# Performance work log

Hardware: AMD Instinct MI355X
Metric: run time of the kernel (lower is better)

## Reference

```python
import jax, jax.numpy as jnp
import numpy as np

B, S, HIDDEN = 2, 2048, 1024
HEADS, HEAD_DIM = 16, 64
GRID_SIZE, SPLINE_ORDER = 5, 3  # efficient-kan defaults


def b_splines(x, grid, k=SPLINE_ORDER):
    """x: (N, in), grid: (in, GRID_SIZE + 2k + 1) -> (N, in, GRID_SIZE + k)."""
    xe = x[..., None]
    bases = ((xe >= grid[:, :-1]) & (xe < grid[:, 1:])).astype(x.dtype)
    for p in range(1, k + 1):  # Cox-de Boor recursion, fixed small loop
        left = (xe - grid[:, : -(p + 1)]) / (grid[:, p:-1] - grid[:, : -(p + 1)]) * bases[..., :-1]
        right = (grid[:, p + 1:] - xe) / (grid[:, p + 1:] - grid[:, 1:-p]) * bases[..., 1:]
        bases = left + right
    return bases


def setup_inputs() -> dict:
    key = jax.random.key(0)
    ks = jax.random.split(key, 7)
    h = 2.0 / GRID_SIZE  # grid_range = [-1, 1]
    grid_1d = (jnp.arange(-SPLINE_ORDER, GRID_SIZE + SPLINE_ORDER + 1, dtype=jnp.float32) * h - 1.0)
    grid = jnp.tile(grid_1d[None, :], (HIDDEN, 1))  # (in, 12)
    return {
        "x": jax.random.normal(ks[0], (B, S, HIDDEN), jnp.float32),
        "base_weight": jax.random.normal(ks[1], (3 * HIDDEN, HIDDEN), jnp.float32) * 0.02,
        "spline_weight": jax.random.normal(ks[2], (3 * HIDDEN, HIDDEN, GRID_SIZE + SPLINE_ORDER), jnp.float32) * 0.02,
        "spline_scaler": jax.random.normal(ks[3], (3 * HIDDEN, HIDDEN), jnp.float32) * 0.1 + 1.0,
        "grid": grid,
        "rotation_matrix": jax.random.normal(ks[4], (HEAD_DIM, HEAD_DIM), jnp.float32) / np.sqrt(HEAD_DIM),
        "out_w": jax.random.normal(ks[5], (HIDDEN, HIDDEN), jnp.float32) * 0.02,
        "out_b": jnp.zeros((HIDDEN,), jnp.float32),
    }


def reference(x, base_weight, spline_weight, spline_scaler, grid, rotation_matrix, out_w, out_b):
    Bc, Sc, Hc = x.shape
    xf = x.reshape(-1, Hc)  # (N, in)
    # KANLinear: silu base branch + B-spline branch
    base = jax.nn.silu(xf) @ base_weight.T  # (N, 3H)
    bs = b_splines(xf, grid)  # (N, in, G+k)
    sw = spline_weight * spline_scaler[..., None]  # scaled spline weight
    spline = bs.reshape(bs.shape[0], -1) @ sw.reshape(sw.shape[0], -1).T
    qkv = (base + spline).reshape(Bc, Sc, HEADS, 3 * HEAD_DIM).transpose(0, 2, 1, 3)
    q, k, v = jnp.split(qkv, 3, axis=-1)  # each (B,H,S,dh)
    # RoPE via full learned rotation matrix
    qr = jnp.einsum('bhsd,md->bhsm', q, rotation_matrix)
    kr = jnp.einsum('bhsd,md->bhsm', k, rotation_matrix)
    scores = jnp.einsum('bhsm,bhtm->bhst', qr, kr) / (HEAD_DIM ** 0.5)
    attn = jax.nn.softmax(scores, axis=-1)
    ctx = jnp.einsum('bhst,bhtd->bhsd', attn, v)
    ctx = ctx.transpose(0, 2, 1, 3).reshape(Bc, Sc, Hc)
    return ctx @ out_w.T + out_b
```

## Files before the change

kernel.cpp:

```cpp
#include <hip/hip_runtime.h>
#include <cstdint>
#include <cstddef>

typedef __bf16 bf16;
typedef bf16  bf16x8 __attribute__((ext_vector_type(8)));
typedef float f32x4  __attribute__((ext_vector_type(4)));

#define GLOBAL_AS __attribute__((address_space(1)))
#define LDS_AS    __attribute__((address_space(3)))

__device__ __forceinline__ void ldg_lds16(const void* g, void* l) {
  __builtin_amdgcn_global_load_lds((const GLOBAL_AS void*)g, (LDS_AS void*)l, 16, 0, 0);
}

constexpr int NB    = 2;
constexpr int SQ    = 2048;
constexpr int HID   = 1024;
constexpr int NHEAD = 16;
constexpr int HD    = 64;
constexpr int NROW  = NB * SQ;
constexpr int KA    = HID + HID * 8;
constexpr int NO    = 3 * HID;

constexpr int NBW = NO * (KA / 8) / 256;
constexpr int NBA = NROW * HID / 256;
constexpr int NBC = HID * HID / 1024;

__global__ __launch_bounds__(256) void prep(const float* __restrict__ X,
                                            const float* __restrict__ Grid,
                                            const float* __restrict__ BW,
                                            const float* __restrict__ SW,
                                            const float* __restrict__ SS,
                                            const float* __restrict__ OW,
                                            bf16* __restrict__ A,
                                            bf16* __restrict__ Wp,
                                            bf16* __restrict__ WOB) {
  const int bx = blockIdx.x, tid = threadIdx.x;
  if (bx < NBW) {
    int idx = bx * 256 + tid;
    int o = idx / 1152;
    int jc = idx - o * 1152;
    float4 f0, f1;
    if (jc < 128) {
      f0 = *(const float4*)(BW + (size_t)o * HID + jc * 8);
      f1 = *(const float4*)(BW + (size_t)o * HID + jc * 8 + 4);
    } else {
      int ii = jc - 128;
      float sc = SS[(size_t)o * HID + ii];
      f0 = *(const float4*)(SW + ((size_t)o * HID + ii) * 8);
      f1 = *(const float4*)(SW + ((size_t)o * HID + ii) * 8 + 4);
      f0.x *= sc; f0.y *= sc; f0.z *= sc; f0.w *= sc;
      f1.x *= sc; f1.y *= sc; f1.z *= sc; f1.w *= sc;
    }
    union { bf16 h[8]; uint4 u; } pk;
    pk.h[0] = (bf16)f0.x; pk.h[1] = (bf16)f0.y; pk.h[2] = (bf16)f0.z; pk.h[3] = (bf16)f0.w;
    pk.h[4] = (bf16)f1.x; pk.h[5] = (bf16)f1.y; pk.h[6] = (bf16)f1.z; pk.h[7] = (bf16)f1.w;
    *(uint4*)(Wp + (size_t)o * KA + jc * 8) = pk.u;
  } else if (bx < NBW + NBA) {
    int idx = (bx - NBW) * 256 + tid;
    int n = idx >> 10, i = idx & 1023;
    float x = X[idx];
    float s = x / (1.0f + __expf(-x));
    A[(size_t)n * KA + i] = (bf16)s;

    float kn[12];
#pragma unroll
    for (int t = 0; t < 12; t++) kn[t] = Grid[t];
    const float inv1 = 1.0f / (kn[1] - kn[0]);
    const float inv2 = 0.5f * inv1;
    const float inv3 = (1.0f / 3.0f) * inv1;
    float bs[11];
#pragma unroll
    for (int t = 0; t < 11; t++) bs[t] = (x >= kn[t] && x < kn[t + 1]) ? 1.0f : 0.0f;
#pragma unroll
    for (int t = 0; t < 10; t++)
      bs[t] = (x - kn[t]) * inv1 * bs[t] + (kn[t + 2] - x) * inv1 * bs[t + 1];
#pragma unroll
    for (int t = 0; t < 9; t++)
      bs[t] = (x - kn[t]) * inv2 * bs[t] + (kn[t + 3] - x) * inv2 * bs[t + 1];
#pragma unroll
    for (int t = 0; t < 8; t++)
      bs[t] = (x - kn[t]) * inv3 * bs[t] + (kn[t + 4] - x) * inv3 * bs[t + 1];
    union { bf16 h[8]; uint4 u; } pk;
#pragma unroll
    for (int t = 0; t < 8; t++) pk.h[t] = (bf16)bs[t];
    *(uint4*)(A + (size_t)n * KA + HID + i * 8) = pk.u;
  } else {
    int i = ((bx - NBW - NBA) * 256 + tid) * 4;
    float4 f = *(const float4*)(OW + i);
    union { bf16 h[4]; uint2 u; } p;
    p.h[0] = (bf16)f.x; p.h[1] = (bf16)f.y; p.h[2] = (bf16)f.z; p.h[3] = (bf16)f.w;
    *(uint2*)(WOB + i) = p.u;
  }
}

__global__ __launch_bounds__(512, 2) void gemm_qkv(const bf16* __restrict__ A,
                                                   const bf16* __restrict__ W,
                                                   bf16* __restrict__ QQ,
                                                   bf16* __restrict__ KK,
                                                   bf16* __restrict__ VV) {
  constexpr int BM = 256, BN = 192, BK = 64;
  constexpr int NT = KA / BK;
  __shared__ __align__(16) bf16 As[2 * BM * BK];
  __shared__ __align__(16) bf16 Bs[2 * BN * BK];
  const int tid  = threadIdx.x;
  const int lane = tid & 63, wave = tid >> 6;
  const int wr = wave >> 2, wc = wave & 3;
  const int l15 = lane & 15, quad = lane >> 4;
  const int xw = l15 & 7;
  const int rowBase = blockIdx.y * BM;
  const int colBase = blockIdx.x * BN;

  int aRow[4], aOff[4];
#pragma unroll
  for (int i = 0; i < 4; i++) {
    int c = i * 512 + tid;
    aRow[i] = c >> 3;
    aOff[i] = ((c & 7) ^ (aRow[i] & 7)) * 8;
  }
  int bRow[3], bOff[3];
#pragma unroll
  for (int i = 0; i < 3; i++) {
    int c = i * 512 + tid;
    bRow[i] = c >> 3;
    bOff[i] = ((c & 7) ^ (bRow[i] & 7)) * 8;
  }
  const int dstBase = tid * 8;

  auto stage = [&](int t, int b) {
    const bf16* Asrc = A + (size_t)rowBase * KA + (size_t)t * BK;
    const bf16* Bsrc = W + (size_t)colBase * KA + (size_t)t * BK;
    bf16* Ad = As + b * (BM * BK);
    bf16* Bd = Bs + b * (BN * BK);
#pragma unroll
    for (int i = 0; i < 4; i++)
      ldg_lds16(Asrc + (size_t)aRow[i] * KA + aOff[i], Ad + i * 4096 + dstBase);
#pragma unroll
    for (int i = 0; i < 3; i++)
      ldg_lds16(Bsrc + (size_t)bRow[i] * KA + bOff[i], Bd + i * 4096 + dstBase);
  };

  f32x4 acc[8][3];
#pragma unroll
  for (int mi = 0; mi < 8; mi++)
#pragma unroll
    for (int nj = 0; nj < 3; nj++) acc[mi][nj] = (f32x4){0.f, 0.f, 0.f, 0.f};

  stage(0, 0);
  stage(1, 1);
  asm volatile("s_waitcnt vmcnt(7)\n\ts_barrier" ::: "memory");

  auto tile_step = [&](int t, int b) {
    const bf16* Ab = As + b * (BM * BK);
    const bf16* Bb = Bs + b * (BN * BK);
    bf16x8 af[2][8], bfv[2][3];
#pragma unroll
    for (int kc = 0; kc < 2; kc++) {
      const int slot = ((kc * 4 + quad) ^ xw) * 8;
#pragma unroll
      for (int mi = 0; mi < 8; mi++)
        af[kc][mi] = *(const bf16x8*)(Ab + (wr * 128 + mi * 16 + l15) * 64 + slot);
#pragma unroll
      for (int nj = 0; nj < 3; nj++)
        bfv[kc][nj] = *(const bf16x8*)(Bb + (wc * 48 + nj * 16 + l15) * 64 + slot);
    }
    __builtin_amdgcn_s_setprio(1);
#pragma unroll
    for (int mi = 0; mi < 8; mi++)
#pragma unroll
      for (int nj = 0; nj < 3; nj++)
        acc[mi][nj] = __builtin_amdgcn_mfma_f32_16x16x32_bf16(af[0][mi], bfv[0][nj], acc[mi][nj], 0, 0, 0);
    __builtin_amdgcn_s_setprio(0);
    asm volatile("s_waitcnt lgkmcnt(0)\n\ts_barrier" ::: "memory");
    if (t + 2 < NT) stage(t + 2, b);
    __builtin_amdgcn_s_setprio(1);
#pragma unroll
    for (int mi = 0; mi < 8; mi++)
#pragma unroll
      for (int nj = 0; nj < 3; nj++)
        acc[mi][nj] = __builtin_amdgcn_mfma_f32_16x16x32_bf16(af[1][mi], bfv[1][nj], acc[mi][nj], 0, 0, 0);
    __builtin_amdgcn_s_setprio(0);
    if (t + 2 < NT)
      asm volatile("s_waitcnt vmcnt(7)\n\ts_barrier" ::: "memory");
    else
      asm volatile("s_waitcnt vmcnt(0)\n\ts_barrier" ::: "memory");
  };

#pragma unroll 1
  for (int t = 0; t < NT; t += 2) {
    tile_step(t, 0);
    tile_step(t + 1, 1);
  }

  const int h = blockIdx.x;
#pragma unroll
  for (int mi = 0; mi < 8; mi++)
#pragma unroll
    for (int nj = 0; nj < 3; nj++)
#pragma unroll
      for (int r = 0; r < 4; r++) {
        int row = rowBase + wr * 128 + mi * 16 + quad * 4 + r;
        int c = wc * 48 + nj * 16 + l15;
        int b = row >> 11, s = row & 2047;
        size_t base = ((size_t)(b * NHEAD + h) * SQ + s) * HD;
        float v = acc[mi][nj][r];
        if (c < 64)        QQ[base + c] = (bf16)v;
        else if (c < 128)  KK[base + c - 64] = (bf16)v;
        else               VV[base + c - 128] = (bf16)v;
      }
}

__global__ __launch_bounds__(256) void trm(const bf16* __restrict__ VV,
                                           bf16* __restrict__ VT,
                                           const float* __restrict__ R,
                                           bf16* __restrict__ Mb) {
  __shared__ __align__(16) char sm[16384];
  const int bx = blockIdx.x, tid = threadIdx.x;
  if (bx < 1024) {
    bf16* Ts = (bf16*)sm;
    const int st = bx & 31, bh = bx >> 5;
    const bf16* src = VV + ((size_t)bh * SQ + st * 64) * HD;
#pragma unroll
    for (int i = 0; i < 2; i++) {
      int c = i * 256 + tid, row = c >> 3, seg = c & 7;
      bf16x8 v8 = *(const bf16x8*)(src + row * HD + seg * 8);
      *(bf16x8*)(&Ts[row * 72 + seg * 8]) = v8;
    }
    __syncthreads();
#pragma unroll
    for (int i = 0; i < 2; i++) {
      int c = i * 256 + tid, drow = c >> 3, seg = c & 7;
      bf16x8 o8;
#pragma unroll
      for (int j = 0; j < 8; j++) o8[j] = Ts[(seg * 8 + j) * 72 + drow];
      *(bf16x8*)(VT + ((size_t)bh * HD + drow) * SQ + st * 64 + seg * 8) = o8;
    }
  } else {
    float* Rl = (float*)sm;
    for (int idx = tid; idx < 4096; idx += 256) Rl[idx] = R[idx];
    __syncthreads();
    int d = tid >> 2;
    int e0 = (tid & 3) * 16;
#pragma unroll
    for (int j = 0; j < 16; j++) {
      int e = e0 + j;
      float acc = 0.f;
#pragma unroll
      for (int m = 0; m < 64; m++) acc += Rl[m * 64 + d] * Rl[m * 64 + e];
      Mb[d * 64 + e] = (bf16)(0.125f * acc);
    }
  }
}

__global__ __launch_bounds__(256) void attn(const bf16* __restrict__ QQ,
                                            const bf16* __restrict__ KK,
                                            const bf16* __restrict__ VT,
                                            const bf16* __restrict__ Mb,
                                            bf16* __restrict__ CTXB) {
  constexpr int NKT = SQ / 64;
  __shared__ __align__(16) bf16 Qs[128 * 64];
  __shared__ __align__(16) bf16 Ks[2 * 64 * 64];
  __shared__ __align__(16) bf16 Vt[2 * 64 * 64];
  __shared__ __align__(16) bf16 Ps[128 * 64];
  __shared__ __align__(16) bf16 Ms[64 * 64];
  const int id  = blockIdx.x;
  const int sub = id >> 3;
  const int bh  = (id & 7) * 4 + (sub >> 4);
  const int qi  = sub & 15;
  const int b = bh >> 4, h = bh & 15;
  const int qbase = qi * 128;
  const bf16* Q  = QQ + (size_t)bh * SQ * HD;
  const bf16* Kp = KK + (size_t)bh * SQ * HD;
  const bf16* Vp = VT + (size_t)bh * HD * SQ;
  const int tid = threadIdx.x, lane = tid & 63, wave = tid >> 6;
  const int l15 = lane & 15, quad = lane >> 4;
  const int sw8 = l15 & 7;
  const float SHIFT = 12.0f;

  auto stageKV = [&](int kt2, int bufsel) {
    const int kb = kt2 * 64;
#pragma unroll
    for (int i = 0; i < 2; i++) {
      int c = i * 256 + tid, row = c >> 3, seg = c & 7;
      ldg_lds16(Kp + (size_t)(kb + row) * HD + ((seg ^ (row & 7)) * 8),
                Ks + bufsel * 4096 + c * 8);
    }
#pragma unroll
    for (int i = 0; i < 2; i++) {
      int c = i * 256 + tid, row = c >> 3, seg = c & 7;
      ldg_lds16(Vp + (size_t)row * SQ + kb + ((seg ^ (row & 7)) * 8),
                Vt + bufsel * 4096 + c * 8);
    }
  };

#pragma unroll
  for (int i = 0; i < 4; i++) {
    int c = i * 256 + tid, row = c >> 3, seg = c & 7;
    ldg_lds16(Q + (size_t)(qbase + row) * HD + ((seg ^ (row & 7)) * 8), Qs + c * 8);
  }
#pragma unroll
  for (int i = 0; i < 2; i++) {
    int c = i * 256 + tid, row = c >> 3, seg = c & 7;
    ldg_lds16(Mb + row * 64 + ((seg ^ (row & 7)) * 8), Ms + c * 8);
  }
  stageKV(0, 0);
  __syncthreads();

  {
    f32x4 racc[2][4];
#pragma unroll
    for (int mi = 0; mi < 2; mi++)
#pragma unroll
      for (int nj = 0; nj < 4; nj++) racc[mi][nj] = (f32x4){0.f, 0.f, 0.f, 0.f};
#pragma unroll
    for (int kc = 0; kc < 2; kc++) {
      const int slot = ((kc * 4 + quad) ^ sw8) * 8;
      bf16x8 aq[2], bm[4];
#pragma unroll
      for (int mi = 0; mi < 2; mi++)
        aq[mi] = *(const bf16x8*)(Qs + (wave * 32 + mi * 16 + l15) * 64 + slot);
#pragma unroll
      for (int nj = 0; nj < 4; nj++)
        bm[nj] = *(const bf16x8*)(Ms + (nj * 16 + l15) * 64 + slot);
#pragma unroll
      for (int mi = 0; mi < 2; mi++)
#pragma unroll
        for (int nj = 0; nj < 4; nj++)
          racc[mi][nj] = __builtin_amdgcn_mfma_f32_16x16x32_bf16(aq[mi], bm[nj], racc[mi][nj], 0, 0, 0);
    }
#pragma unroll
    for (int mi = 0; mi < 2; mi++)
#pragma unroll
      for (int nj = 0; nj < 4; nj++)
#pragma unroll
        for (int r = 0; r < 4; r++) {
          int qrow = wave * 32 + mi * 16 + quad * 4 + r;
          int slot = ((nj * 2 + (l15 >> 3)) ^ (qrow & 7)) * 8 + (l15 & 7);
          Qs[qrow * 64 + slot] = (bf16)racc[mi][nj][r];
        }
  }
  bf16x8 qf[2][2];
#pragma unroll
  for (int kc = 0; kc < 2; kc++)
#pragma unroll
    for (int mi = 0; mi < 2; mi++)
      qf[mi][kc] = *(const bf16x8*)(Qs + (wave * 32 + mi * 16 + l15) * 64 + (((kc * 4 + quad) ^ sw8) * 8));

  float lpart[2][4];
  f32x4 ctxacc[2][4];
#pragma unroll
  for (int mi = 0; mi < 2; mi++)
#pragma unroll
    for (int r = 0; r < 4; r++) lpart[mi][r] = 0.f;
#pragma unroll
  for (int mi = 0; mi < 2; mi++)
#pragma unroll
    for (int nd = 0; nd < 4; nd++) ctxacc[mi][nd] = (f32x4){0.f, 0.f, 0.f, 0.f};

#pragma unroll 1
  for (int kt = 0; kt < NKT; kt++) {
    const int buf = kt & 1;
    const bf16* Kb = Ks + buf * 4096;
    const bf16* Vb = Vt + buf * 4096;
    if (kt + 1 < NKT) stageKV(kt + 1, buf ^ 1);

    f32x4 sacc[2][4];
#pragma unroll
    for (int mi = 0; mi < 2; mi++)
#pragma unroll
      for (int nj = 0; nj < 4; nj++) sacc[mi][nj] = (f32x4){0.f, 0.f, 0.f, 0.f};
#pragma unroll
    for (int kc = 0; kc < 2; kc++) {
      const int slot = ((kc * 4 + quad) ^ sw8) * 8;
      bf16x8 bfr[4];
#pragma unroll
      for (int nj = 0; nj < 4; nj++)
        bfr[nj] = *(const bf16x8*)(Kb + (nj * 16 + l15) * 64 + slot);
#pragma unroll
      for (int mi = 0; mi < 2; mi++)
#pragma unroll
        for (int nj = 0; nj < 4; nj++)
          sacc[mi][nj] = __builtin_amdgcn_mfma_f32_16x16x32_bf16(qf[mi][kc], bfr[nj], sacc[mi][nj], 0, 0, 0);
    }
#pragma unroll
    for (int mi = 0; mi < 2; mi++)
#pragma unroll
      for (int nj = 0; nj < 4; nj++)
#pragma unroll
        for (int r = 0; r < 4; r++) {
          float p = __expf(sacc[mi][nj][r] - SHIFT);
          lpart[mi][r] += p;
          int prow = wave * 32 + mi * 16 + quad * 4 + r;
          int slot = ((nj * 2 + (l15 >> 3)) ^ (prow & 7)) * 8 + (l15 & 7);
          Ps[prow * 64 + slot] = (bf16)p;
        }
#pragma unroll
    for (int kc = 0; kc < 2; kc++) {
      const int slot = ((kc * 4 + quad) ^ sw8) * 8;
      bf16x8 af[2], bfr[4];
#pragma unroll
      for (int mi = 0; mi < 2; mi++)
        af[mi] = *(const bf16x8*)(Ps + (wave * 32 + mi * 16 + l15) * 64 + slot);
#pragma unroll
      for (int nd = 0; nd < 4; nd++)
        bfr[nd] = *(const bf16x8*)(Vb + (nd * 16 + l15) * 64 + slot);
#pragma unroll
      for (int mi = 0; mi < 2; mi++)
#pragma unroll
        for (int nd = 0; nd < 4; nd++)
          ctxacc[mi][nd] = __builtin_amdgcn_mfma_f32_16x16x32_bf16(af[mi], bfr[nd], ctxacc[mi][nd], 0, 0, 0);
    }
    asm volatile("s_waitcnt vmcnt(0)\n\ts_barrier" ::: "memory");
  }

#pragma unroll
  for (int mi = 0; mi < 2; mi++)
#pragma unroll
    for (int r = 0; r < 4; r++) {
      float l = lpart[mi][r];
#pragma unroll
      for (int off = 1; off < 16; off <<= 1) l += __shfl_xor(l, off);
      float inv = 1.0f / l;
#pragma unroll
      for (int nd = 0; nd < 4; nd++) {
        int srow = qbase + wave * 32 + mi * 16 + quad * 4 + r;
        float val = ctxacc[mi][nd][r] * inv;
        CTXB[(size_t)(b * SQ + srow) * HID + h * HD + nd * 16 + l15] = (bf16)val;
      }
    }
}

__global__ __launch_bounds__(256) void gemm_out(const bf16* __restrict__ CTX,
                                                const bf16* __restrict__ WOB,
                                                const float* __restrict__ OB,
                                                float* __restrict__ OUT) {
  constexpr int K = HID, NIT = K / 32;
  __shared__ __align__(16) bf16 As[2 * 128 * 32];
  __shared__ __align__(16) bf16 Bs[2 * 128 * 32];
  const int tid  = threadIdx.x;
  const int lane = tid & 63, wave = tid >> 6;
  const int wm = (wave >> 1) * 64, wn = (wave & 1) * 64;
  const int l15 = lane & 15, quad = lane >> 4;
  const int rA = tid >> 2;
  const int swSrc = ((tid & 3) ^ ((rA >> 1) & 3)) * 8;
  const int swRd  = (quad ^ ((l15 >> 1) & 3)) * 8;
  const int rowBase = blockIdx.y * 128, colBase = blockIdx.x * 128;

  const bf16* Ag1 = CTX + (size_t)(rowBase + rA) * K + swSrc;
  const bf16* Ag2 = CTX + (size_t)(rowBase + 64 + rA) * K + swSrc;
  const bf16* Bg1 = WOB + (size_t)(colBase + rA) * K + swSrc;
  const bf16* Bg2 = WOB + (size_t)(colBase + 64 + rA) * K + swSrc;

  auto stage = [&](int it, int b) {
    const int k0 = it * 32;
    ldg_lds16(Ag1 + k0, As + b * 4096 + tid * 8);
    ldg_lds16(Ag2 + k0, As + b * 4096 + 2048 + tid * 8);
    ldg_lds16(Bg1 + k0, Bs + b * 4096 + tid * 8);
    ldg_lds16(Bg2 + k0, Bs + b * 4096 + 2048 + tid * 8);
  };

  f32x4 acc[4][4];
#pragma unroll
  for (int mi = 0; mi < 4; mi++)
#pragma unroll
    for (int ni = 0; ni < 4; ni++) acc[mi][ni] = (f32x4){0.f, 0.f, 0.f, 0.f};

  stage(0, 0);
  asm volatile("s_waitcnt vmcnt(0)\n\ts_barrier" ::: "memory");

#pragma unroll 1
  for (int it = 0; it < NIT; it++) {
    const int buf = it & 1;
    if (it + 1 < NIT) stage(it + 1, buf ^ 1);
    bf16x8 af[4], bfr[4];
#pragma unroll
    for (int mi = 0; mi < 4; mi++)
      af[mi] = *(const bf16x8*)(As + buf * 4096 + (wm + mi * 16 + l15) * 32 + swRd);
#pragma unroll
    for (int ni = 0; ni < 4; ni++)
      bfr[ni] = *(const bf16x8*)(Bs + buf * 4096 + (wn + ni * 16 + l15) * 32 + swRd);
#pragma unroll
    for (int mi = 0; mi < 4; mi++)
#pragma unroll
      for (int ni = 0; ni < 4; ni++)
        acc[mi][ni] = __builtin_amdgcn_mfma_f32_16x16x32_bf16(af[mi], bfr[ni], acc[mi][ni], 0, 0, 0);
    asm volatile("s_waitcnt vmcnt(0)\n\ts_barrier" ::: "memory");
  }

#pragma unroll
  for (int mi = 0; mi < 4; mi++)
#pragma unroll
    for (int ni = 0; ni < 4; ni++)
#pragma unroll
      for (int r = 0; r < 4; r++) {
        int row = rowBase + wm + mi * 16 + quad * 4 + r;
        int col = colBase + wn + ni * 16 + l15;
        OUT[(size_t)row * HID + col] = acc[mi][ni][r] + OB[col];
      }
}

extern "C" void kernel_launch(void* const* d_in, const int* in_sizes, int n_in,
                              void* d_out, int out_size, void* d_ws, size_t ws_size,
                              hipStream_t stream) {
  const float* x    = (const float*)d_in[0];
  const float* bw   = (const float*)d_in[1];
  const float* sw   = (const float*)d_in[2];
  const float* ss   = (const float*)d_in[3];
  const float* grid = (const float*)d_in[4];
  const float* rot  = (const float*)d_in[5];
  const float* ow   = (const float*)d_in[6];
  const float* ob   = (const float*)d_in[7];
  float* out = (float*)d_out;

  char* ws = (char*)d_ws;
  bf16* Aact = (bf16*)(ws);
  bf16* vt   = (bf16*)(ws);
  bf16* Mb   = (bf16*)(ws + 8388608);
  bf16* Wp   = (bf16*)(ws + 75497472);
  bf16* qq   = (bf16*)(ws + 132120576);
  bf16* kk   = (bf16*)(ws + 140509184);
  bf16* vv   = (bf16*)(ws + 148897792);
  bf16* ctxb = (bf16*)(ws + 157286400);
  bf16* wob  = (bf16*)(ws + 165675008);

  prep<<<NBW + NBA + NBC, 256, 0, stream>>>(x, grid, bw, sw, ss, ow, Aact, Wp, wob);
  gemm_qkv<<<dim3(NO / 192, NROW / 256), 512, 0, stream>>>(Aact, Wp, qq, kk, vv);
  trm<<<1025, 256, 0, stream>>>(vv, vt, rot, Mb);
  attn<<<512, 256, 0, stream>>>(qq, kk, vt, Mb, ctxb);
  gemm_out<<<dim3(HID / 128, NROW / 128), 256, 0, stream>>>(ctxb, wob, ob, out);
}
```

Measured before the change: 526.3 us.

## Fuse V transpose into QKV GEMM epilogue and fold rotation prep into prep kernel

The separate transpose/rotation kernel is removed. The QKV GEMM epilogue now writes V directly in transposed layout with packed 4-element stores, and the R^T R matrix is computed by an extra block in the prep kernel, stored temporarily in the output buffer. The GEMM tile changes from 256x192 with 512 threads to 128x192 with 256 threads, which doubles the block count. This saves a launch and a round trip of V through memory, but the transposed V stores are strided, and the smaller tile lowers A-reuse per block.

```diff
diff --git a/kernel.cpp b/kernel.cpp
--- a/kernel.cpp
+++ b/kernel.cpp
@@ -32,9 +32,12 @@
                                             const float* __restrict__ SW,
                                             const float* __restrict__ SS,
                                             const float* __restrict__ OW,
+                                            const float* __restrict__ R,
                                             bf16* __restrict__ A,
                                             bf16* __restrict__ Wp,
-                                            bf16* __restrict__ WOB) {
+                                            bf16* __restrict__ WOB,
+                                            bf16* __restrict__ Mb) {
+  __shared__ float Rl[64 * 64];
   const int bx = blockIdx.x, tid = threadIdx.x;
   if (bx < NBW) {
     int idx = bx * 256 + tid;
@@ -85,27 +88,40 @@
 #pragma unroll
     for (int t = 0; t < 8; t++) pk.h[t] = (bf16)bs[t];
     *(uint4*)(A + (size_t)n * KA + HID + i * 8) = pk.u;
-  } else {
+  } else if (bx < NBW + NBA + NBC) {
     int i = ((bx - NBW - NBA) * 256 + tid) * 4;
     float4 f = *(const float4*)(OW + i);
     union { bf16 h[4]; uint2 u; } p;
     p.h[0] = (bf16)f.x; p.h[1] = (bf16)f.y; p.h[2] = (bf16)f.z; p.h[3] = (bf16)f.w;
     *(uint2*)(WOB + i) = p.u;
+  } else {
+    for (int idx = tid; idx < 4096; idx += 256) Rl[idx] = R[idx];
+    __syncthreads();
+    int d = tid >> 2;
+    int e0 = (tid & 3) * 16;
+#pragma unroll
+    for (int j = 0; j < 16; j++) {
+      int e = e0 + j;
+      float acc = 0.f;
+#pragma unroll
+      for (int m = 0; m < 64; m++) acc += Rl[m * 64 + d] * Rl[m * 64 + e];
+      Mb[d * 64 + e] = (bf16)(0.125f * acc);
+    }
   }
 }
 
-__global__ __launch_bounds__(512, 2) void gemm_qkv(const bf16* __restrict__ A,
+__global__ __launch_bounds__(256, 2) void gemm_qkv(const bf16* __restrict__ A,
                                                    const bf16* __restrict__ W,
                                                    bf16* __restrict__ QQ,
                                                    bf16* __restrict__ KK,
-                                                   bf16* __restrict__ VV) {
-  constexpr int BM = 256, BN = 192, BK = 64;
+                                                   bf16* __restrict__ VT) {
+  constexpr int BM = 128, BN = 192, BK = 64;
   constexpr int NT = KA / BK;
   __shared__ __align__(16) bf16 As[2 * BM * BK];
   __shared__ __align__(16) bf16 Bs[2 * BN * BK];
   const int tid  = threadIdx.x;
   const int lane = tid & 63, wave = tid >> 6;
-  const int wr = wave >> 2, wc = wave & 3;
+  const int wr = wave >> 1, wc = wave & 1;
   const int l15 = lane & 15, quad = lane >> 4;
   const int xw = l15 & 7;
   const int rowBase = blockIdx.y * BM;
@@ -114,14 +130,14 @@
   int aRow[4], aOff[4];
 #pragma unroll
   for (int i = 0; i < 4; i++) {
-    int c = i * 512 + tid;
+    int c = i * 256 + tid;
     aRow[i] = c >> 3;
     aOff[i] = ((c & 7) ^ (aRow[i] & 7)) * 8;
   }
-  int bRow[3], bOff[3];
-#pragma unroll
-  for (int i = 0; i < 3; i++) {
-    int c = i * 512 + tid;
+  int bRow[6], bOff[6];
+#pragma unroll
+  for (int i = 0; i < 6; i++) {
+    int c = i * 256 + tid;
     bRow[i] = c >> 3;
     bOff[i] = ((c & 7) ^ (bRow[i] & 7)) * 8;
   }
@@ -134,54 +150,54 @@
     bf16* Bd = Bs + b * (BN * BK);
 #pragma unroll
     for (int i = 0; i < 4; i++)
-      ldg_lds16(Asrc + (size_t)aRow[i] * KA + aOff[i], Ad + i * 4096 + dstBase);
-#pragma unroll
-    for (int i = 0; i < 3; i++)
-      ldg_lds16(Bsrc + (size_t)bRow[i] * KA + bOff[i], Bd + i * 4096 + dstBase);
+      ldg_lds16(Asrc + (size_t)aRow[i] * KA + aOff[i], Ad + i * 2048 + dstBase);
+#pragma unroll
+    for (int i = 0; i < 6; i++)
+      ldg_lds16(Bsrc + (size_t)bRow[i] * KA + bOff[i], Bd + i * 2048 + dstBase);
   };
 
-  f32x4 acc[8][3];
-#pragma unroll
-  for (int mi = 0; mi < 8; mi++)
-#pragma unroll
-    for (int nj = 0; nj < 3; nj++) acc[mi][nj] = (f32x4){0.f, 0.f, 0.f, 0.f};
+  f32x4 acc[4][6];
+#pragma unroll
+  for (int mi = 0; mi < 4; mi++)
+#pragma unroll
+    for (int nj = 0; nj < 6; nj++) acc[mi][nj] = (f32x4){0.f, 0.f, 0.f, 0.f};
 
   stage(0, 0);
   stage(1, 1);
-  asm volatile("s_waitcnt vmcnt(7)\n\ts_barrier" ::: "memory");
+  asm volatile("s_waitcnt vmcnt(10)\n\ts_barrier" ::: "memory");
 
   auto tile_step = [&](int t, int b) {
     const bf16* Ab = As + b * (BM * BK);
     const bf16* Bb = Bs + b * (BN * BK);
-    bf16x8 af[2][8], bfv[2][3];
+    bf16x8 af[2][4], bfv[2][6];
 #pragma unroll
     for (int kc = 0; kc < 2; kc++) {
       const int slot = ((kc * 4 + quad) ^ xw) * 8;
 #pragma unroll
-      for (int mi = 0; mi < 8; mi++)
-        af[kc][mi] = *(const bf16x8*)(Ab + (wr * 128 + mi * 16 + l15) * 64 + slot);
-#pragma unroll
-      for (int nj = 0; nj < 3; nj++)
-        bfv[kc][nj] = *(const bf16x8*)(Bb + (wc * 48 + nj * 16 + l15) * 64 + slot);
+      for (int mi = 0; mi < 4; mi++)
+        af[kc][mi] = *(const bf16x8*)(Ab + (wr * 64 + mi * 16 + l15) * 64 + slot);
+#pragma unroll
+      for (int nj = 0; nj < 6; nj++)
+        bfv[kc][nj] = *(const bf16x8*)(Bb + (wc * 96 + nj * 16 + l15) * 64 + slot);
     }
     __builtin_amdgcn_s_setprio(1);
 #pragma unroll
-    for (int mi = 0; mi < 8; mi++)
-#pragma unroll
-      for (int nj = 0; nj < 3; nj++)
+    for (int mi = 0; mi < 4; mi++)
+#pragma unroll
+      for (int nj = 0; nj < 6; nj++)
         acc[mi][nj] = __builtin_amdgcn_mfma_f32_16x16x32_bf16(af[0][mi], bfv[0][nj], acc[mi][nj], 0, 0, 0);
     __builtin_amdgcn_s_setprio(0);
     asm volatile("s_waitcnt lgkmcnt(0)\n\ts_barrier" ::: "memory");
     if (t + 2 < NT) stage(t + 2, b);
     __builtin_amdgcn_s_setprio(1);
 #pragma unroll
-    for (int mi = 0; mi < 8; mi++)
-#pragma unroll
-      for (int nj = 0; nj < 3; nj++)
+    for (int mi = 0; mi < 4; mi++)
+#pragma unroll
+      for (int nj = 0; nj < 6; nj++)
         acc[mi][nj] = __builtin_amdgcn_mfma_f32_16x16x32_bf16(af[1][mi], bfv[1][nj], acc[mi][nj], 0, 0, 0);
     __builtin_amdgcn_s_setprio(0);
     if (t + 2 < NT)
-      asm volatile("s_waitcnt vmcnt(7)\n\ts_barrier" ::: "memory");
+      asm volatile("s_waitcnt vmcnt(10)\n\ts_barrier" ::: "memory");
     else
       asm volatile("s_waitcnt vmcnt(0)\n\ts_barrier" ::: "memory");
   };
@@ -194,62 +210,25 @@
 
   const int h = blockIdx.x;
 #pragma unroll
-  for (int mi = 0; mi < 8; mi++)
-#pragma unroll
-    for (int nj = 0; nj < 3; nj++)
-#pragma unroll
-      for (int r = 0; r < 4; r++) {
-        int row = rowBase + wr * 128 + mi * 16 + quad * 4 + r;
-        int c = wc * 48 + nj * 16 + l15;
-        int b = row >> 11, s = row & 2047;
-        size_t base = ((size_t)(b * NHEAD + h) * SQ + s) * HD;
-        float v = acc[mi][nj][r];
-        if (c < 64)        QQ[base + c] = (bf16)v;
-        else if (c < 128)  KK[base + c - 64] = (bf16)v;
-        else               VV[base + c - 128] = (bf16)v;
+  for (int mi = 0; mi < 4; mi++)
+#pragma unroll
+    for (int nj = 0; nj < 6; nj++) {
+      int c = wc * 96 + nj * 16 + l15;
+      int row0 = rowBase + wr * 64 + mi * 16 + quad * 4;
+      int bb = row0 >> 11, s0 = row0 & 2047;
+      if (c < 128) {
+        size_t base = ((size_t)(bb * NHEAD + h) * SQ + s0) * HD;
+        bf16* dst = (c < 64) ? (QQ + base + c) : (KK + base + c - 64);
+#pragma unroll
+        for (int r = 0; r < 4; r++) dst[(size_t)r * HD] = (bf16)acc[mi][nj][r];
+      } else {
+        int d = c - 128;
+        union { bf16 hh[4]; uint2 u; } pk;
+#pragma unroll
+        for (int r = 0; r < 4; r++) pk.hh[r] = (bf16)acc[mi][nj][r];
+        *(uint2*)(VT + ((size_t)(bb * NHEAD + h) * HD + d) * SQ + s0) = pk.u;
       }
-}
-
-__global__ __launch_bounds__(256) void trm(const bf16* __restrict__ VV,
-                                           bf16* __restrict__ VT,
-                                           const float* __restrict__ R,
-                                           bf16* __restrict__ Mb) {
-  __shared__ __align__(16) char sm[16384];
-  const int bx = blockIdx.x, tid = threadIdx.x;
-  if (bx < 1024) {
-    bf16* Ts = (bf16*)sm;
-    const int st = bx & 31, bh = bx >> 5;
-    const bf16* src = VV + ((size_t)bh * SQ + st * 64) * HD;
-#pragma unroll
-    for (int i = 0; i < 2; i++) {
-      int c = i * 256 + tid, row = c >> 3, seg = c & 7;
-      bf16x8 v8 = *(const bf16x8*)(src + row * HD + seg * 8);
-      *(bf16x8*)(&Ts[row * 72 + seg * 8]) = v8;
-    }
-    __syncthreads();
-#pragma unroll
-    for (int i = 0; i < 2; i++) {
-      int c = i * 256 + tid, drow = c >> 3, seg = c & 7;
-      bf16x8 o8;
-#pragma unroll
-      for (int j = 0; j < 8; j++) o8[j] = Ts[(seg * 8 + j) * 72 + drow];
-      *(bf16x8*)(VT + ((size_t)bh * HD + drow) * SQ + st * 64 + seg * 8) = o8;
-    }
-  } else {
-    float* Rl = (float*)sm;
-    for (int idx = tid; idx < 4096; idx += 256) Rl[idx] = R[idx];
-    __syncthreads();
-    int d = tid >> 2;
-    int e0 = (tid & 3) * 16;
-#pragma unroll
-    for (int j = 0; j < 16; j++) {
-      int e = e0 + j;
-      float acc = 0.f;
-#pragma unroll
-      for (int m = 0; m < 64; m++) acc += Rl[m * 64 + d] * Rl[m * 64 + e];
-      Mb[d * 64 + e] = (bf16)(0.125f * acc);
-    }
-  }
+    }
 }
 
 __global__ __launch_bounds__(256) void attn(const bf16* __restrict__ QQ,
@@ -514,18 +493,16 @@
 
   char* ws = (char*)d_ws;
   bf16* Aact = (bf16*)(ws);
-  bf16* vt   = (bf16*)(ws);
-  bf16* Mb   = (bf16*)(ws + 8388608);
   bf16* Wp   = (bf16*)(ws + 75497472);
   bf16* qq   = (bf16*)(ws + 132120576);
   bf16* kk   = (bf16*)(ws + 140509184);
-  bf16* vv   = (bf16*)(ws + 148897792);
+  bf16* vt   = (bf16*)(ws + 148897792);
   bf16* ctxb = (bf16*)(ws + 157286400);
   bf16* wob  = (bf16*)(ws + 165675008);
-
-  prep<<<NBW + NBA + NBC, 256, 0, stream>>>(x, grid, bw, sw, ss, ow, Aact, Wp, wob);
-  gemm_qkv<<<dim3(NO / 192, NROW / 256), 512, 0, stream>>>(Aact, Wp, qq, kk, vv);
-  trm<<<1025, 256, 0, stream>>>(vv, vt, rot, Mb);
+  bf16* Mb   = (bf16*)out;
+
+  prep<<<NBW + NBA + NBC + 1, 256, 0, stream>>>(x, grid, bw, sw, ss, ow, rot, Aact, Wp, wob, Mb);
+  gemm_qkv<<<dim3(NO / 192, NROW / 128), 256, 0, stream>>>(Aact, Wp, qq, kk, vt);
   attn<<<512, 256, 0, stream>>>(qq, kk, vt, Mb, ctxb);
   gemm_out<<<dim3(HID / 128, NROW / 128), 256, 0, stream>>>(ctxb, wob, ob, out);
 }
```

Result: slower. 640.2 us (+21.6%).
